# Kernel optimization log

Measured on AMD Instinct MI355X. Metric: run time of the kernel, lower is better.

The kernel has to match this reference:

```python
import jax, jax.numpy as jnp
import numpy as np

N = 100000   # nodes
E = 1200000  # edges
NIN, EIN = 6, 1
HID, L, H = 64, 3, 4
D = HID // H  # 16 per-head dim


def setup_inputs() -> dict:
    key = jax.random.key(0)
    ks = jax.random.split(key, 20)
    r = lambda k, shape: (jax.random.normal(k, shape, dtype=jnp.float32) * 0.1)
    inp = {
        "x": jax.random.normal(ks[0], (N, NIN), dtype=jnp.float32),
        "edge_index": jax.random.randint(ks[1], (2, E), 0, N, dtype=jnp.int64),
        "edge_attr": jax.random.normal(ks[2], (E, EIN), dtype=jnp.float32),
        # node encoder (Linear-ReLU-Linear)
        "w_ne1": r(ks[3], (NIN, HID)), "b_ne1": jnp.zeros((HID,), jnp.float32),
        "w_ne2": r(ks[4], (HID, HID)), "b_ne2": jnp.zeros((HID,), jnp.float32),
        # edge encoder (Linear)
        "w_ee": r(ks[5], (EIN, HID)), "b_ee": jnp.zeros((HID,), jnp.float32),
        # stacked GAT layers (PyG GATConv w/ edge features, concat heads)
        "w_gat": r(ks[6], (L, HID, HID)),      # node lin per layer
        "w_eg": r(ks[7], (L, HID, HID)),       # edge lin per layer
        "att_src": r(ks[8], (L, H, D)),
        "att_dst": r(ks[9], (L, H, D)),
        "att_edge": r(ks[10], (L, H, D)),
        "b_gat": jnp.zeros((L, HID), jnp.float32),
        # per-layer LayerNorm
        "ln_g": jnp.ones((L, HID), jnp.float32),
        "ln_b": jnp.zeros((L, HID), jnp.float32),
        # output projection
        "w_out": r(ks[11], (HID, HID)), "b_out": jnp.zeros((HID,), jnp.float32),
    }
    return inp


def _layernorm(x, g, b, eps=1e-5):
    m = jnp.mean(x, axis=-1, keepdims=True)
    v = jnp.mean(jnp.square(x - m), axis=-1, keepdims=True)
    return (x - m) * jax.lax.rsqrt(v + eps) * g + b


def reference(x, edge_index, edge_attr, w_ne1, b_ne1, w_ne2, b_ne2, w_ee, b_ee,
              w_gat, w_eg, att_src, att_dst, att_edge, b_gat, ln_g, ln_b,
              w_out, b_out):
    n = x.shape[0]
    src, dst = edge_index[0], edge_index[1]
    # encode nodes / edges
    h = jax.nn.relu(x @ w_ne1 + b_ne1) @ w_ne2 + b_ne2          # [N, HID]
    e = edge_attr @ w_ee + b_ee                                  # [E, HID]
    num_layers = w_gat.shape[0]
    for l in range(num_layers):
        hw = (h @ w_gat[l]).reshape(n, H, D)                     # [N,H,D]
        ew = (e @ w_eg[l]).reshape(-1, H, D)                     # [E,H,D]
        a_s = jnp.sum(hw * att_src[l], axis=-1)                  # [N,H]
        a_d = jnp.sum(hw * att_dst[l], axis=-1)                  # [N,H]
        a_e = jnp.sum(ew * att_edge[l], axis=-1)                 # [E,H]
        score = jax.nn.leaky_relu(a_s[src] + a_d[dst] + a_e, 0.2)  # [E,H]
        # softmax over incoming edges of each destination node
        smax = jax.ops.segment_max(score, dst, num_segments=n)
        ex = jnp.exp(score - smax[dst])
        den = jax.ops.segment_sum(ex, dst, num_segments=n)
        alpha = ex / (den[dst] + 1e-16)                          # [E,H]
        msg = alpha[:, :, None] * hw[src]                        # [E,H,D]
        agg = jax.ops.segment_sum(msg, dst, num_segments=n)      # [N,H,D]
        agg = agg.reshape(n, H * D) + b_gat[l]
        h = _layernorm(h + jax.nn.elu(agg), ln_g[l], ln_b[l])
    return h @ w_out + b_out
```

## Files before the change

kernel.cpp:

```cpp
#include <hip/hip_runtime.h>

#define NIN 6
#define HIDN 64
#define NHEAD 4
#define DEGPAD 5

__device__ __forceinline__ unsigned short f2bf(float f) {
    unsigned u = __float_as_uint(f);
    unsigned r = (u >> 16) & 1u;
    return (unsigned short)((u + 0x7fffu + r) >> 16);
}

__device__ __forceinline__ void mm64_plain_body(
    const float* __restrict__ src, const float* __restrict__ W,
    const float* __restrict__ bias, float* __restrict__ dst, int N,
    int wv0, int nw) {
    int j = threadIdx.x & 63;
    float Wc[HIDN];
#pragma unroll
    for (int k = 0; k < HIDN; k++) Wc[k] = W[k * HIDN + j];
    float bj = bias[j];
    for (int n0 = wv0; n0 < N; n0 += nw) {
        int n = __builtin_amdgcn_readfirstlane(n0);
        const float4* __restrict__ row = (const float4*)(src + (size_t)n * HIDN);
        float a0 = 0.f, a1 = 0.f, a2 = 0.f, a3 = 0.f;
#pragma unroll
        for (int kk = 0; kk < 16; kk++) {
            float4 r = row[kk];
            a0 += r.x * Wc[4 * kk];
            a1 += r.y * Wc[4 * kk + 1];
            a2 += r.z * Wc[4 * kk + 2];
            a3 += r.w * Wc[4 * kk + 3];
        }
        dst[(size_t)n * HIDN + j] = ((a0 + a1) + (a2 + a3)) + bj;
    }
}

__device__ __forceinline__ void mm64_attn_body(
    const float* __restrict__ src, const float* __restrict__ W,
    const float* __restrict__ att_s, const float* __restrict__ att_d,
    unsigned short* __restrict__ dst16,
    float* __restrict__ a_s, float* __restrict__ a_d, int N,
    int wv0, int nw) {
    int j = threadIdx.x & 63;
    float Wc[HIDN];
#pragma unroll
    for (int k = 0; k < HIDN; k++) Wc[k] = W[k * HIDN + j];
    float asj = att_s[j];
    float adj = att_d[j];
    for (int n0 = wv0; n0 < N; n0 += nw) {
        int n = __builtin_amdgcn_readfirstlane(n0);
        const float4* __restrict__ row = (const float4*)(src + (size_t)n * HIDN);
        float a0 = 0.f, a1 = 0.f, a2 = 0.f, a3 = 0.f;
#pragma unroll
        for (int kk = 0; kk < 16; kk++) {
            float4 r = row[kk];
            a0 += r.x * Wc[4 * kk];
            a1 += r.y * Wc[4 * kk + 1];
            a2 += r.z * Wc[4 * kk + 2];
            a3 += r.w * Wc[4 * kk + 3];
        }
        float acc = (a0 + a1) + (a2 + a3);
        dst16[(size_t)n * HIDN + j] = f2bf(acc);
        float ts = acc * asj;
        float td = acc * adj;
#pragma unroll
        for (int o = 8; o > 0; o >>= 1) {
            ts += __shfl_xor(ts, o);
            td += __shfl_xor(td, o);
        }
        if ((j & 15) == 0) {
            a_s[(size_t)n * NHEAD + (j >> 4)] = ts;
            a_d[(size_t)n * NHEAD + (j >> 4)] = td;
        }
    }
}

__global__ __launch_bounds__(256) void pre_kernel(
    const int* __restrict__ ei, unsigned* __restrict__ deg,
    unsigned* __restrict__ rank, int E,
    const float* __restrict__ x, const float* __restrict__ w1,
    const float* __restrict__ b1, float* __restrict__ hid, int N,
    const float* __restrict__ w_ee, const float* __restrict__ b_ee,
    const float* __restrict__ w_eg, const float* __restrict__ att_edge,
    float* __restrict__ c1, float* __restrict__ c0,
    int histBlocks, int encBlocks) {
    int b = blockIdx.x;
    if (b < histBlocks) {
        int e = b * 256 + threadIdx.x;
        if (e < E) rank[e] = atomicAdd(&deg[(size_t)ei[E + e] << DEGPAD], 1u);
        return;
    }
    b -= histBlocks;
    if (b < encBlocks) {
        int t = b * 256 + threadIdx.x;
        int n = t >> 6, j = t & 63;
        if (n >= N) return;
        float acc = b1[j];
#pragma unroll
        for (int i = 0; i < NIN; i++) acc += x[n * NIN + i] * w1[i * HIDN + j];
        hid[(size_t)n * HIDN + j] = acc > 0.f ? acc : 0.f;
        return;
    }
    int w = threadIdx.x >> 6, j = threadIdx.x & 63;
    for (int p = w; p < 12; p += 4) {
        int l = p >> 2, hh = p & 3;
        const float* wr = w_eg + l * 4096 + j * 64 + hh * 16;
        const float* ae = att_edge + l * 64 + hh * 16;
        float wj = 0.f;
#pragma unroll
        for (int d = 0; d < 16; d++) wj += wr[d] * ae[d];
        float s1 = w_ee[j] * wj;
        float s0 = b_ee[j] * wj;
#pragma unroll
        for (int o = 32; o > 0; o >>= 1) {
            s1 += __shfl_xor(s1, o);
            s0 += __shfl_xor(s0, o);
        }
        if (j == 0) { c1[l * 4 + hh] = s1; c0[l * 4 + hh] = s0; }
    }
}

__global__ __launch_bounds__(256) void mid_kernel(
    const unsigned* __restrict__ deg, unsigned* __restrict__ rp,
    unsigned* __restrict__ bsum, int N,
    const float* __restrict__ src, const float* __restrict__ W,
    const float* __restrict__ bias, float* __restrict__ dst,
    int scanBlocks, int mmWaves) {
    __shared__ unsigned sm[256];
    int b = blockIdx.x;
    if (b < scanBlocks) {
        int t = threadIdx.x, i = b * 256 + t;
        unsigned v = (i < N) ? deg[(size_t)i << DEGPAD] : 0u;
        sm[t] = v;
        __syncthreads();
        unsigned xx = v;
        for (int o = 1; o < 256; o <<= 1) {
            unsigned add = (t >= o) ? sm[t - o] : 0u;
            __syncthreads();
            xx += add; sm[t] = xx;
            __syncthreads();
        }
        if (i < N) rp[i] = xx - v;
        if (t == 255) bsum[b] = xx;
        return;
    }
    int wv0 = ((b - scanBlocks) * 256 + threadIdx.x) >> 6;
    mm64_plain_body(src, W, bias, dst, N, wv0, mmWaves);
}

__global__ __launch_bounds__(256) void scan23_kernel(
    unsigned* __restrict__ rp, const unsigned* __restrict__ bsum,
    int N, int E) {
    __shared__ unsigned red[256];
    int b = blockIdx.x, t = threadIdx.x;
    unsigned partial = 0;
    for (int j = t; j < b; j += 256) partial += bsum[j];
    red[t] = partial;
    __syncthreads();
    for (int o = 128; o > 0; o >>= 1) {
        if (t < o) red[t] += red[t + o];
        __syncthreads();
    }
    unsigned off = red[0];
    int i = b * 256 + t;
    if (i < N) rp[i] += off;
    if (b == 0 && t == 0) rp[N] = (unsigned)E;
}

__global__ __launch_bounds__(256) void sca_kernel(
    const int* __restrict__ ei, const float* __restrict__ eattr,
    const unsigned* __restrict__ rp, const unsigned* __restrict__ rank,
    int2* __restrict__ eca, int E,
    const float* __restrict__ src, const float* __restrict__ W,
    const float* __restrict__ att_s, const float* __restrict__ att_d,
    unsigned short* __restrict__ dst16,
    float* __restrict__ a_s, float* __restrict__ a_d, int N,
    int scatBlocks, int mmWaves) {
    int b = blockIdx.x;
    if (b < scatBlocks) {
        int e = b * 256 + threadIdx.x;
        if (e >= E) return;
        int s = ei[e], d = ei[E + e];
        unsigned p = rp[d] + rank[e];
        eca[p] = make_int2(s, __float_as_int(eattr[e]));
        return;
    }
    int wv0 = ((b - scatBlocks) * 256 + threadIdx.x) >> 6;
    mm64_attn_body(src, W, att_s, att_d, dst16, a_s, a_d, N, wv0, mmWaves);
}

template <int MODE>
__global__ __launch_bounds__(256) void gat_fused_x_kernel(
    const unsigned* __restrict__ rp, const int2* __restrict__ eca,
    const unsigned short* __restrict__ hw16,
    const float* __restrict__ a_s, const float* __restrict__ a_d,
    const float* __restrict__ c1, const float* __restrict__ c0,
    float* __restrict__ h, const float* __restrict__ bg,
    const float* __restrict__ g, const float* __restrict__ b, int N,
    const float* __restrict__ Wnext,
    const float* __restrict__ att_s_w, const float* __restrict__ att_d_w,
    const float* __restrict__ bias_out,
    unsigned short* __restrict__ hw16_out,
    float* __restrict__ a_s_out, float* __restrict__ a_d_out,
    float* __restrict__ out) {
    __shared__ float WgL[4096];
    __shared__ float exl[4 * 272];
    __shared__ int srl[4 * 68];

    {
        const float4* __restrict__ Wn4 = (const float4*)Wnext;
        float4* WgL4 = (float4*)WgL;
        for (int i = threadIdx.x; i < 1024; i += 256) WgL4[i] = Wn4[i];
    }
    __syncthreads();

    int t = blockIdx.x * blockDim.x + threadIdx.x;
    int lane = t & 63;
    int q = lane >> 4;
    int l = lane & 15;
    int hd = l >> 2;
    int sub = l & 3;
    int n = ((t >> 6) << 2) + q;
    int wslot = (threadIdx.x >> 6);
    float* myex = exl + wslot * 272 + 68 * q;
    int* mysrc = srl + wslot * 68 + 17 * q;

    bool nv = n < N;
    unsigned beg = nv ? rp[n] : 0u;
    int deg = nv ? (int)(rp[n + 1] - beg) : 0;

    float4 ad4 = nv ? *(const float4*)(a_d + ((size_t)n << 2)) : make_float4(0, 0, 0, 0);
    float4 C1 = *(const float4*)c1;
    float4 C0 = *(const float4*)c0;

    int md = deg;
    md = max(md, __shfl_xor(md, 16));
    md = max(md, __shfl_xor(md, 32));
    int chunks = (md + 15) >> 4;

    const unsigned* __restrict__ hwp = (const unsigned*)hw16;
    unsigned loff = (unsigned)(l << 1);

    float ssum = 0.f;
    float ac0 = 0.f, ac1 = 0.f, ac2 = 0.f, ac3 = 0.f;

    for (int k = 0; k < chunks; k++) {
        int i = (k << 4) + l;
        bool act = i < deg;
        int2 ce = act ? eca[beg + i] : make_int2(0, 0);
        int src = ce.x;
        float ea = __int_as_float(ce.y);
        float4 as4 = act ? *(const float4*)(a_s + ((size_t)src << 2))
                         : make_float4(0, 0, 0, 0);
        float s0 = as4.x + ad4.x + ea * C1.x + C0.x;
        float s1 = as4.y + ad4.y + ea * C1.y + C0.y;
        float s2 = as4.z + ad4.z + ea * C1.z + C0.z;
        float s3 = as4.w + ad4.w + ea * C1.w + C0.w;
        s0 = s0 >= 0.f ? s0 : 0.2f * s0;
        s1 = s1 >= 0.f ? s1 : 0.2f * s1;
        s2 = s2 >= 0.f ? s2 : 0.2f * s2;
        s3 = s3 >= 0.f ? s3 : 0.2f * s3;
        float e0 = act ? __expf(s0) : 0.f;
        float e1 = act ? __expf(s1) : 0.f;
        float e2 = act ? __expf(s2) : 0.f;
        float e3 = act ? __expf(s3) : 0.f;
        *(float4*)(myex + (l << 2)) = make_float4(e0, e1, e2, e3);
        mysrc[l] = act ? src : 0;

        float w0 = myex[(sub << 2) + hd];
        float w1 = myex[((sub + 4) << 2) + hd];
        float w2 = myex[((sub + 8) << 2) + hd];
        float w3 = myex[((sub + 12) << 2) + hd];
        float csum = (w0 + w1) + (w2 + w3);
        csum += __shfl_xor(csum, 1);
        csum += __shfl_xor(csum, 2);
        ssum += csum;

#pragma unroll
        for (int e = 0; e < 16; e++) {
            float w = myex[(e << 2) + hd];
            int so = mysrc[e];
            uint2 uu = *(const uint2*)(hwp + (((unsigned)so << 5) + loff));
            ac0 += w * __uint_as_float(uu.x << 16);
            ac1 += w * __uint_as_float(uu.x & 0xffff0000u);
            ac2 += w * __uint_as_float(uu.y << 16);
            ac3 += w * __uint_as_float(uu.y & 0xffff0000u);
        }
    }

    float inv = 1.f / (ssum + 1e-16f);
    float4 bg4 = *(const float4*)(bg + (l << 2));
    float4 hv4 = nv ? *(const float4*)(h + (size_t)n * HIDN + (l << 2))
                    : make_float4(0, 0, 0, 0);

    float a0 = ac0 * inv + bg4.x;
    float a1 = ac1 * inv + bg4.y;
    float a2 = ac2 * inv + bg4.z;
    float a3 = ac3 * inv + bg4.w;
    a0 = a0 > 0.f ? a0 : (__expf(a0) - 1.f);
    a1 = a1 > 0.f ? a1 : (__expf(a1) - 1.f);
    a2 = a2 > 0.f ? a2 : (__expf(a2) - 1.f);
    a3 = a3 > 0.f ? a3 : (__expf(a3) - 1.f);
    float v0 = hv4.x + a0, v1 = hv4.y + a1, v2 = hv4.z + a2, v3 = hv4.w + a3;

    float s = (v0 + v1) + (v2 + v3);
    float sq = (v0 * v0 + v1 * v1) + (v2 * v2 + v3 * v3);
#pragma unroll
    for (int o = 8; o > 0; o >>= 1) {
        s += __shfl_xor(s, o);
        sq += __shfl_xor(sq, o);
    }
    float mean = s * (1.f / 64.f);
    float var = sq * (1.f / 64.f) - mean * mean;
    float rr = rsqrtf(var + 1e-5f);
    float4 g4 = *(const float4*)(g + (l << 2));
    float4 b4 = *(const float4*)(b + (l << 2));
    v0 = (v0 - mean) * rr * g4.x + b4.x;
    v1 = (v1 - mean) * rr * g4.y + b4.y;
    v2 = (v2 - mean) * rr * g4.z + b4.z;
    v3 = (v3 - mean) * rr * g4.w + b4.w;

    if (MODE == 0 && nv) {
        *(float4*)(h + (size_t)n * HIDN + (l << 2)) = make_float4(v0, v1, v2, v3);
    }

    float* stg = exl + wslot * 272;
    *(float4*)(stg + (q << 6) + (l << 2)) = make_float4(v0, v1, v2, v3);

    float4 A0 = make_float4(0, 0, 0, 0), A1 = make_float4(0, 0, 0, 0);
    float4 A2 = make_float4(0, 0, 0, 0), A3 = make_float4(0, 0, 0, 0);
#pragma unroll
    for (int kk = 0; kk < 16; kk++) {
        float4 hk = *(const float4*)(stg + (q << 6) + (kk << 2));
        const float* wr = WgL + (kk << 8) + (l << 2);
        float4 w0 = *(const float4*)(wr);
        float4 w1 = *(const float4*)(wr + 64);
        float4 w2 = *(const float4*)(wr + 128);
        float4 w3 = *(const float4*)(wr + 192);
        A0.x += hk.x * w0.x; A0.y += hk.x * w0.y; A0.z += hk.x * w0.z; A0.w += hk.x * w0.w;
        A1.x += hk.y * w1.x; A1.y += hk.y * w1.y; A1.z += hk.y * w1.z; A1.w += hk.y * w1.w;
        A2.x += hk.z * w2.x; A2.y += hk.z * w2.y; A2.z += hk.z * w2.z; A2.w += hk.z * w2.w;
        A3.x += hk.w * w3.x; A3.y += hk.w * w3.y; A3.z += hk.w * w3.z; A3.w += hk.w * w3.w;
    }
    float o0 = (A0.x + A1.x) + (A2.x + A3.x);
    float o1 = (A0.y + A1.y) + (A2.y + A3.y);
    float o2 = (A0.z + A1.z) + (A2.z + A3.z);
    float o3 = (A0.w + A1.w) + (A2.w + A3.w);

    if (MODE == 0) {
        if (nv) {
            ushort4 pk = make_ushort4(f2bf(o0), f2bf(o1), f2bf(o2), f2bf(o3));
            *(ushort4*)(hw16_out + (size_t)n * HIDN + (l << 2)) = pk;
        }
        float4 asw = *(const float4*)(att_s_w + (l << 2));
        float4 adw = *(const float4*)(att_d_w + (l << 2));
        float ts = (o0 * asw.x + o1 * asw.y) + (o2 * asw.z + o3 * asw.w);
        float td = (o0 * adw.x + o1 * adw.y) + (o2 * adw.z + o3 * adw.w);
        ts += __shfl_xor(ts, 1); ts += __shfl_xor(ts, 2);
        td += __shfl_xor(td, 1); td += __shfl_xor(td, 2);
        if (nv && (l & 3) == 0) {
            a_s_out[(size_t)n * NHEAD + (l >> 2)] = ts;
            a_d_out[(size_t)n * NHEAD + (l >> 2)] = td;
        }
    } else {
        if (nv) {
            float4 bo = *(const float4*)(bias_out + (l << 2));
            *(float4*)(out + (size_t)n * HIDN + (l << 2)) =
                make_float4(o0 + bo.x, o1 + bo.y, o2 + bo.z, o3 + bo.w);
        }
    }
}

extern "C" void kernel_launch(void* const* d_in, const int* in_sizes, int n_in,
                              void* d_out, int out_size, void* d_ws, size_t ws_size,
                              hipStream_t stream) {
    const float* x      = (const float*)d_in[0];
    const int*   ei     = (const int*)d_in[1];
    const float* eattr  = (const float*)d_in[2];
    const float* w_ne1  = (const float*)d_in[3];
    const float* b_ne1  = (const float*)d_in[4];
    const float* w_ne2  = (const float*)d_in[5];
    const float* b_ne2  = (const float*)d_in[6];
    const float* w_ee   = (const float*)d_in[7];
    const float* b_ee   = (const float*)d_in[8];
    const float* w_gat  = (const float*)d_in[9];
    const float* w_eg   = (const float*)d_in[10];
    const float* att_src= (const float*)d_in[11];
    const float* att_dst= (const float*)d_in[12];
    const float* att_edge=(const float*)d_in[13];
    const float* b_gat  = (const float*)d_in[14];
    const float* ln_g   = (const float*)d_in[15];
    const float* ln_b   = (const float*)d_in[16];
    const float* w_out  = (const float*)d_in[17];
    const float* b_out  = (const float*)d_in[18];

    const int N = in_sizes[0] / NIN;
    const int E = in_sizes[2];

    float* ws   = (float*)d_ws;
    float* h    = ws;
    float* hid  = h + (size_t)N * 64;
    unsigned short* hw16 = (unsigned short*)(hid + (size_t)N * 64);
    float* a_s  = (float*)(hw16 + (size_t)N * 64);
    float* a_d  = a_s + (size_t)N * 4;
    float* c1   = a_d + (size_t)N * 4;
    float* c0   = c1 + 12;
    int2*  eca  = (int2*)(c0 + 12);
    unsigned* rank = (unsigned*)(eca + (size_t)E);
    unsigned* deg  = rank + (size_t)E;
    unsigned* rp   = deg + ((size_t)N << DEGPAD);
    unsigned* bsum = rp + (size_t)N + 1;

    unsigned short* hw16b = (unsigned short*)hid;
    float* a_sb = (float*)(hw16b + (size_t)N * 64);
    float* a_db = a_sb + (size_t)N * 4;

    dim3 blk(256);
    int edgeBlocks = (E + 255) / 256;
    int encBlocks  = (int)(((size_t)N * 64 + 255) / 256);
    int quadBlocks = (int)(((size_t)((N + 3) / 4) * 64 + 255) / 256);
    int nodeBlocks = (N + 255) / 256;
    int mmBlocks = 2048;
    int mmWaves  = mmBlocks * 4;

    hipMemsetAsync(deg, 0, ((size_t)N << DEGPAD) * sizeof(unsigned), stream);

    pre_kernel<<<edgeBlocks + encBlocks + 1, blk, 0, stream>>>(
        ei, deg, rank, E,
        x, w_ne1, b_ne1, hid, N,
        w_ee, b_ee, w_eg, att_edge, c1, c0,
        edgeBlocks, encBlocks);

    mid_kernel<<<nodeBlocks + mmBlocks, blk, 0, stream>>>(
        deg, rp, bsum, N, hid, w_ne2, b_ne2, h, nodeBlocks, mmWaves);

    scan23_kernel<<<nodeBlocks, blk, 0, stream>>>(rp, bsum, N, E);

    sca_kernel<<<edgeBlocks + mmBlocks, blk, 0, stream>>>(
        ei, eattr, rp, rank, eca, E,
        h, w_gat, att_src, att_dst, hw16, a_s, a_d, N,
        edgeBlocks, mmWaves);

    gat_fused_x_kernel<0><<<quadBlocks, blk, 0, stream>>>(
        rp, eca, hw16, a_s, a_d, c1 + 0, c0 + 0,
        h, b_gat + 0, ln_g + 0, ln_b + 0, N,
        w_gat + (size_t)1 * 4096, att_src + 64, att_dst + 64, nullptr,
        hw16b, a_sb, a_db, nullptr);

    gat_fused_x_kernel<0><<<quadBlocks, blk, 0, stream>>>(
        rp, eca, hw16b, a_sb, a_db, c1 + 4, c0 + 4,
        h, b_gat + 64, ln_g + 64, ln_b + 64, N,
        w_gat + (size_t)2 * 4096, att_src + 2 * 64, att_dst + 2 * 64, nullptr,
        hw16, a_s, a_d, nullptr);

    gat_fused_x_kernel<1><<<quadBlocks, blk, 0, stream>>>(
        rp, eca, hw16, a_s, a_d, c1 + 8, c0 + 8,
        h, b_gat + 2 * 64, ln_g + 2 * 64, ln_b + 2 * 64, N,
        w_out, nullptr, nullptr, b_out,
        nullptr, nullptr, nullptr, (float*)d_out);
}
```

Before: 429.6 us.

## Fuse block scan into single-pass decoupled look-back, drop separate scan kernel

Replaces the two-pass row-pointer prefix scan (per-block scan plus a second kernel adding block offsets) with a single-pass decoupled look-back scan inside mid_kernel, using tagged status words and agent-scope atomics. This removes one kernel launch and the extra pass over rp. It also pre-shifts source indices when staging them in shared memory, and adds a minimum-blocks-per-CU launch bound to the GAT kernel. The look-back relies on earlier blocks making forward progress, and the occupancy hint may force register spills.

```diff
diff --git a/kernel.cpp b/kernel.cpp
--- a/kernel.cpp
+++ b/kernel.cpp
@@ -123,13 +123,14 @@
 
 __global__ __launch_bounds__(256) void mid_kernel(
     const unsigned* __restrict__ deg, unsigned* __restrict__ rp,
-    unsigned* __restrict__ bsum, int N,
+    unsigned* __restrict__ st, int N, int E,
     const float* __restrict__ src, const float* __restrict__ W,
     const float* __restrict__ bias, float* __restrict__ dst,
     int scanBlocks, int mmWaves) {
-    __shared__ unsigned sm[256];
     int b = blockIdx.x;
     if (b < scanBlocks) {
+        __shared__ unsigned sm[256];
+        __shared__ unsigned s_prefix;
         int t = threadIdx.x, i = b * 256 + t;
         unsigned v = (i < N) ? deg[(size_t)i << DEGPAD] : 0u;
         sm[t] = v;
@@ -141,31 +142,54 @@
             xx += add; sm[t] = xx;
             __syncthreads();
         }
-        if (i < N) rp[i] = xx - v;
-        if (t == 255) bsum[b] = xx;
+        if (t == 255) {
+            unsigned tag = (b == 0) ? (2u << 30) : (1u << 30);
+            __hip_atomic_store(&st[b], tag | xx, __ATOMIC_RELEASE,
+                               __HIP_MEMORY_SCOPE_AGENT);
+        }
+        if (b == 0) {
+            if (t == 0) s_prefix = 0u;
+        } else if (t < 64) {
+            unsigned pfx = 0u;
+            int base = b - 1;
+            for (;;) {
+                int j = base - t;
+                unsigned s;
+                for (;;) {
+                    s = (j >= 0) ? __hip_atomic_load(&st[j], __ATOMIC_ACQUIRE,
+                                                     __HIP_MEMORY_SCOPE_AGENT)
+                                 : (2u << 30);
+                    if (__all((s >> 30) != 0u)) break;
+                }
+                unsigned long long m2 = __ballot((s >> 30) == 2u);
+                if (m2 != 0ull) {
+                    int k = __ffsll(m2) - 1;
+                    unsigned val = (t <= k) ? (s & 0x3fffffffu) : 0u;
+#pragma unroll
+                    for (int o = 32; o > 0; o >>= 1) val += __shfl_xor(val, o);
+                    pfx += val;
+                    break;
+                } else {
+                    unsigned val = (j >= 0) ? (s & 0x3fffffffu) : 0u;
+#pragma unroll
+                    for (int o = 32; o > 0; o >>= 1) val += __shfl_xor(val, o);
+                    pfx += val;
+                    base -= 64;
+                }
+            }
+            if (t == 0) {
+                s_prefix = pfx;
+                __hip_atomic_store(&st[b], (2u << 30) | (pfx + sm[255]),
+                                   __ATOMIC_RELEASE, __HIP_MEMORY_SCOPE_AGENT);
+            }
+        }
+        __syncthreads();
+        if (i < N) rp[i] = (xx - v) + s_prefix;
+        if (i == N - 1) rp[N] = (unsigned)E;
         return;
     }
     int wv0 = ((b - scanBlocks) * 256 + threadIdx.x) >> 6;
     mm64_plain_body(src, W, bias, dst, N, wv0, mmWaves);
-}
-
-__global__ __launch_bounds__(256) void scan23_kernel(
-    unsigned* __restrict__ rp, const unsigned* __restrict__ bsum,
-    int N, int E) {
-    __shared__ unsigned red[256];
-    int b = blockIdx.x, t = threadIdx.x;
-    unsigned partial = 0;
-    for (int j = t; j < b; j += 256) partial += bsum[j];
-    red[t] = partial;
-    __syncthreads();
-    for (int o = 128; o > 0; o >>= 1) {
-        if (t < o) red[t] += red[t + o];
-        __syncthreads();
-    }
-    unsigned off = red[0];
-    int i = b * 256 + t;
-    if (i < N) rp[i] += off;
-    if (b == 0 && t == 0) rp[N] = (unsigned)E;
 }
 
 __global__ __launch_bounds__(256) void sca_kernel(
@@ -191,7 +215,7 @@
 }
 
 template <int MODE>
-__global__ __launch_bounds__(256) void gat_fused_x_kernel(
+__global__ __launch_bounds__(256, 7) void gat_fused_x_kernel(
     const unsigned* __restrict__ rp, const int2* __restrict__ eca,
     const unsigned short* __restrict__ hw16,
     const float* __restrict__ a_s, const float* __restrict__ a_d,
@@ -266,7 +290,7 @@
         float e2 = act ? __expf(s2) : 0.f;
         float e3 = act ? __expf(s3) : 0.f;
         *(float4*)(myex + (l << 2)) = make_float4(e0, e1, e2, e3);
-        mysrc[l] = act ? src : 0;
+        mysrc[l] = act ? (src << 5) : 0;
 
         float w0 = myex[(sub << 2) + hd];
         float w1 = myex[((sub + 4) << 2) + hd];
@@ -280,8 +304,8 @@
 #pragma unroll
         for (int e = 0; e < 16; e++) {
             float w = myex[(e << 2) + hd];
-            int so = mysrc[e];
-            uint2 uu = *(const uint2*)(hwp + (((unsigned)so << 5) + loff));
+            unsigned so = (unsigned)mysrc[e];
+            uint2 uu = *(const uint2*)(hwp + (so + loff));
             ac0 += w * __uint_as_float(uu.x << 16);
             ac1 += w * __uint_as_float(uu.x & 0xffff0000u);
             ac2 += w * __uint_as_float(uu.y << 16);
@@ -409,8 +433,8 @@
     int2*  eca  = (int2*)(c0 + 12);
     unsigned* rank = (unsigned*)(eca + (size_t)E);
     unsigned* deg  = rank + (size_t)E;
-    unsigned* rp   = deg + ((size_t)N << DEGPAD);
-    unsigned* bsum = rp + (size_t)N + 1;
+    unsigned* st   = deg + ((size_t)N << DEGPAD);
+    unsigned* rp   = st + 1024;
 
     unsigned short* hw16b = (unsigned short*)hid;
     float* a_sb = (float*)(hw16b + (size_t)N * 64);
@@ -424,7 +448,7 @@
     int mmBlocks = 2048;
     int mmWaves  = mmBlocks * 4;
 
-    hipMemsetAsync(deg, 0, ((size_t)N << DEGPAD) * sizeof(unsigned), stream);
+    hipMemsetAsync(deg, 0, (((size_t)N << DEGPAD) + 1024) * sizeof(unsigned), stream);
 
     pre_kernel<<<edgeBlocks + encBlocks + 1, blk, 0, stream>>>(
         ei, deg, rank, E,
@@ -433,9 +457,7 @@
         edgeBlocks, encBlocks);
 
     mid_kernel<<<nodeBlocks + mmBlocks, blk, 0, stream>>>(
-        deg, rp, bsum, N, hid, w_ne2, b_ne2, h, nodeBlocks, mmWaves);
-
-    scan23_kernel<<<nodeBlocks, blk, 0, stream>>>(rp, bsum, N, E);
+        deg, rp, st, N, E, hid, w_ne2, b_ne2, h, nodeBlocks, mmWaves);
 
     sca_kernel<<<edgeBlocks + mmBlocks, blk, 0, stream>>>(
         ei, eattr, rp, rank, eca, E,
```

After: 843.0 us. 96.2% more time.
